# Kernel optimization log

Hardware: AMD Instinct MI355X
Metric: run time of the kernel (lower is better)

Reference implementation:

```python
import math
import jax, jax.numpy as jnp
import numpy as np

B, L, DIM, H = 2, 2048, 1024, 16
D = DIM // H  # head_dim = 64
EPS = 1e-6


def setup_inputs() -> dict:
    key = jax.random.key(0)
    ks = jax.random.split(key, 5)
    s = 0.02
    return {
        "x": jax.random.normal(ks[0], (B, L, DIM), jnp.float32),
        "pe": jax.random.normal(ks[1], (B, 1, L, D // 2, 2, 2), jnp.float32),
        "w_qkv": jax.random.normal(ks[2], (DIM, 3 * DIM), jnp.float32) * s,
        "q_scale": jnp.ones((D,), jnp.float32),
        "k_scale": jnp.ones((D,), jnp.float32),
        "w_proj": jax.random.normal(ks[3], (DIM, DIM), jnp.float32) * s,
        "b_proj": jnp.zeros((DIM,), jnp.float32),
    }


def _rmsnorm(t, scale):
    # flax nnx.RMSNorm: x * rsqrt(mean(x^2) + eps) * scale, over last dim
    var = jnp.mean(jnp.square(t), axis=-1, keepdims=True)
    return t * jax.lax.rsqrt(var + EPS) * scale


def _apply_rope(t, pe):
    # t: [B,H,L,D]; pe: [B,1,L,D/2,2,2]
    t2 = t.reshape(*t.shape[:-1], D // 2, 1, 2)
    out = pe[..., 0] * t2[..., 0] + pe[..., 1] * t2[..., 1]  # [B,H,L,D/2,2]
    return out.reshape(t.shape)


def reference(x, pe, w_qkv, q_scale, k_scale, w_proj, b_proj):
    # fused QKV projection
    qkv = jnp.einsum('bld,de->ble', x, w_qkv)  # [B,L,3*DIM]
    qkv = qkv.reshape(B, L, 3, H, D).transpose(2, 0, 3, 1, 4)  # [3,B,H,L,D]
    q, k, v = qkv[0], qkv[1], qkv[2]
    # QK RMSNorm
    q = _rmsnorm(q, q_scale)
    k = _rmsnorm(k, k_scale)
    # RoPE via pe
    q = _apply_rope(q, pe)
    k = _apply_rope(k, pe)
    # scaled dot product attention
    scores = jnp.einsum('bhqd,bhkd->bhqk', q, k) / math.sqrt(D)
    attn = jax.nn.softmax(scores, axis=-1)
    o = jnp.einsum('bhqk,bhkd->bhqd', attn, v)  # [B,H,L,D]
    o = o.transpose(0, 2, 1, 3).reshape(B, L, DIM)  # B H L D -> B L (H D)
    # output projection
    return jnp.einsum('bld,de->ble', o, w_proj) + b_proj
```

## Files before the change

### kernel.cpp

```cpp
#include <hip/hip_runtime.h>
#include <math.h>

#define BB 2
#define LL 2048
#define DIMM 1024
#define HH 16
#define DD 64
#define QKV_N 3072

typedef unsigned short u16;
typedef unsigned int u32;
typedef __attribute__((ext_vector_type(8))) short short8;
typedef __attribute__((ext_vector_type(4))) float f32x4;

__device__ __forceinline__ float bf2f(u16 h) {
    unsigned u = ((unsigned)h) << 16;
    return __uint_as_float(u);
}
__device__ __forceinline__ u16 f2bf(float f) {
    unsigned u = __float_as_uint(f);
    u += 0x7fffu + ((u >> 16) & 1u);
    return (u16)(u >> 16);
}
__device__ __forceinline__ u32 pack_bf2(float lo, float hi) {
    u32 a = __float_as_uint(hi) + 0x8000u;
    u32 b = __float_as_uint(lo) + 0x8000u;
    return __builtin_amdgcn_perm(a, b, 0x07060302u);
}
__device__ __forceinline__ void gload16(const u16* g, u16* l) {
    __builtin_amdgcn_global_load_lds(
        (const __attribute__((address_space(1))) void*)g,
        (__attribute__((address_space(3))) void*)l, 16, 0, 0);
}

__global__ __launch_bounds__(256) void convx(
    const float* __restrict__ X, u16* __restrict__ Xb)
{
    int i = (blockIdx.x * 256 + threadIdx.x) * 8;
    float4 a = *(const float4*)&X[i];
    float4 b = *(const float4*)&X[i + 4];
    u16 t[8] = {f2bf(a.x), f2bf(a.y), f2bf(a.z), f2bf(a.w),
                f2bf(b.x), f2bf(b.y), f2bf(b.z), f2bf(b.w)};
    *(uint4*)&Xb[i] = *(uint4*)t;
}

__global__ __launch_bounds__(256) void convt(
    const float* __restrict__ W, u16* __restrict__ Wt, int K, int N)
{
    __shared__ u16 s[64][72];
    const int tid = threadIdx.x;
    const int k0 = blockIdx.x * 64, n0 = blockIdx.y * 64;
#pragma unroll
    for (int t = 0; t < 16; ++t) {
        int flat = t * 256 + tid;
        int kk = flat >> 6, nn = flat & 63;
        s[nn][kk] = f2bf(W[(size_t)(k0 + kk) * N + n0 + nn]);
    }
    __syncthreads();
#pragma unroll
    for (int t = 0; t < 2; ++t) {
        int chunk = t * 256 + tid;
        int nn = chunk >> 3, kc = chunk & 7;
        *(uint4*)&Wt[(size_t)(n0 + nn) * K + k0 + kc * 8] = *(uint4*)&s[nn][kc * 8];
    }
}

__global__ __launch_bounds__(256) void gemm_qkv(
    const u16* __restrict__ A, const u16* __restrict__ Bt,
    u16* __restrict__ C, u16* __restrict__ kp, u16* __restrict__ vp,
    const float* __restrict__ pe,
    const float* __restrict__ qs, const float* __restrict__ ks)
{
    __shared__ u16 smem[2 * 16384];

    const int tid = threadIdx.x;
    const int wave = tid >> 6, lane = tid & 63;
    const int mIdx = lane & 15, quad = lane >> 4;
    const int wr = wave >> 1, wc = wave & 1;
    const int xcd = blockIdx.x & 7, lid = blockIdx.x >> 3;
    const int m0 = ((xcd & 3) * 8 + (lid & 7)) * 128;
    const int n0 = ((xcd >> 2) * 12 + (lid >> 3)) * 128;
    const int N = QKV_N, K = DIMM;
    const int lr = lane >> 3, lc = lane & 7;

    f32x4 acc[4][4];
#pragma unroll
    for (int a = 0; a < 4; ++a)
#pragma unroll
        for (int b = 0; b < 4; ++b) acc[a][b] = (f32x4){0.f, 0.f, 0.f, 0.f};

    auto stage = [&](int buf, int k0) {
        u16* sA = smem + buf * 16384;
        u16* sB = sA + 8192;
#pragma unroll
        for (int j = 0; j < 4; ++j) {
            int r0 = 32 * wave + 8 * j + lr;
            int kc = 8 * (lc ^ lr);
            gload16(&A[(size_t)(m0 + r0) * K + k0 + kc], &sA[(32 * wave + 8 * j) * 64]);
            gload16(&Bt[(size_t)(n0 + r0) * K + k0 + kc], &sB[(32 * wave + 8 * j) * 64]);
        }
    };

    stage(0, 0);
    __syncthreads();
    int cur = 0;
    for (int t = 0; t < 16; ++t) {
        if (t + 1 < 16) stage(cur ^ 1, (t + 1) * 64);
        const u16* sA = smem + cur * 16384;
        const u16* sB = sA + 8192;
#pragma unroll
        for (int ks2 = 0; ks2 < 2; ++ks2) {
            short8 af[4], bfr[4];
#pragma unroll
            for (int mt = 0; mt < 4; ++mt) {
                int Ra = 64 * wr + 16 * mt + mIdx;
                af[mt] = *(const short8*)&sA[Ra * 64 + 8 * ((ks2 * 4 + quad) ^ (Ra & 7))];
            }
#pragma unroll
            for (int nt = 0; nt < 4; ++nt) {
                int Rb = 64 * wc + 16 * nt + mIdx;
                bfr[nt] = *(const short8*)&sB[Rb * 64 + 8 * ((ks2 * 4 + quad) ^ (Rb & 7))];
            }
#pragma unroll
            for (int mt = 0; mt < 4; ++mt)
#pragma unroll
                for (int nt = 0; nt < 4; ++nt)
                    acc[mt][nt] = __builtin_amdgcn_mfma_f32_16x16x32_bf16(
                        af[mt], bfr[nt], acc[mt][nt], 0, 0, 0);
        }
        __syncthreads();
        cur ^= 1;
    }

    if (n0 >= 2048) {
#pragma unroll
        for (int mt = 0; mt < 4; ++mt) {
            const int tl0 = 64 * wr + 16 * mt + 4 * quad;
#pragma unroll
            for (int nt = 0; nt < 4; ++nt) {
                const int d = 16 * nt + mIdx;
                const int lblk = ((wc * 2 + (tl0 >> 6)) * 4 + (d >> 4)) * 2
                                 + ((tl0 >> 5) & 1);
                const int ln = (d & 15) + 16 * ((tl0 >> 3) & 3);
                uint2 pr;
                pr.x = pack_bf2(acc[mt][nt][0], acc[mt][nt][1]);
                pr.y = pack_bf2(acc[mt][nt][2], acc[mt][nt][3]);
                *(uint2*)&smem[lblk * 512 + ln * 8 + (tl0 & 7)] = pr;
            }
        }
        __syncthreads();
        {
            const int b = m0 >> 11;
            const int h0 = (n0 - 2048) >> 6;
            const int ktb = (m0 & 2047) >> 6;
#pragma unroll
            for (int g2 = 0; g2 < 4; ++g2) {
                const int bh = b * 16 + h0 + (g2 >> 1);
                const int kt = ktb + (g2 & 1);
                u16* dst = vp + ((size_t)(bh * 32 + kt) * 8) * 512;
                const u16* src = &smem[g2 * 8 * 512];
#pragma unroll
                for (int ps = 0; ps < 2; ++ps) {
                    const int off = (ps * 256 + tid) * 8;
                    *(uint4*)&dst[off] = *(const uint4*)&src[off];
                }
            }
        }
    } else {
        const bool isq = (n0 < 1024);
        const float* scv = isq ? qs : ks;
        const float pre = isq ? 0.18033688011112042f : 1.0f;
        float scl[4];
#pragma unroll
        for (int nt = 0; nt < 4; ++nt) scl[nt] = scv[16 * nt + mIdx];

#pragma unroll
        for (int mt = 0; mt < 4; ++mt) {
#pragma unroll
            for (int r = 0; r < 4; ++r) {
                float s = 0.f;
#pragma unroll
                for (int nt = 0; nt < 4; ++nt) {
                    float a = acc[mt][nt][r];
                    s += a * a;
                }
                s += __shfl_xor(s, 1);
                s += __shfl_xor(s, 2);
                s += __shfl_xor(s, 4);
                s += __shfl_xor(s, 8);
                float rn = rsqrtf(s * (1.f / 64.f) + 1e-6f);
                const int tl = 64 * wr + 16 * mt + 4 * quad + r;
                const int R = m0 + tl;
                size_t peo = (size_t)R * 128;
#pragma unroll
                for (int nt = 0; nt < 4; ++nt) {
                    float v = acc[mt][nt][r] * rn * scl[nt];
                    float pp = __shfl_xor(v, 1);
                    float2 pw = *(const float2*)&pe[peo + 2 * (16 * nt + mIdx)];
                    float e  = (mIdx & 1) ? pp : v;
                    float od = (mIdx & 1) ? v : pp;
                    u16 val = f2bf((pw.x * e + pw.y * od) * pre);
                    if (isq) {
                        C[(size_t)R * N + n0 + 64 * wc + 16 * nt + mIdx] = val;
                    } else {
                        const int d = 16 * nt + mIdx;
                        const int lblk = ((wc * 2 + (tl >> 6)) * 4 + ((tl >> 4) & 3)) * 2
                                         + (d >> 5);
                        smem[lblk * 512 + ((tl & 15) + 16 * ((d >> 3) & 3)) * 8
                             + (d & 7)] = val;
                    }
                }
            }
        }
        if (!isq) {
            __syncthreads();
            const int b = m0 >> 11;
            const int h0 = (n0 - 1024) >> 6;
            const int ktb = (m0 & 2047) >> 6;
#pragma unroll
            for (int g2 = 0; g2 < 4; ++g2) {
                const int bh = b * 16 + h0 + (g2 >> 1);
                const int kt = ktb + (g2 & 1);
                u16* dst = kp + ((size_t)(bh * 32 + kt) * 8) * 512;
                const u16* src = &smem[g2 * 8 * 512];
#pragma unroll
                for (int ps = 0; ps < 2; ++ps) {
                    const int off = (ps * 256 + tid) * 8;
                    *(uint4*)&dst[off] = *(const uint4*)&src[off];
                }
            }
        }
    }
}

__global__ __launch_bounds__(256) void gemm_proj(
    const u16* __restrict__ A, const u16* __restrict__ Bt,
    const float* __restrict__ bias, float* __restrict__ C)
{
    __shared__ u16 smem[2 * 12288];

    const int tid = threadIdx.x;
    const int wave = tid >> 6, lane = tid & 63;
    const int mIdx = lane & 15, quad = lane >> 4;
    const int wr = wave >> 1, wc = wave & 1;
    const int xcd = blockIdx.x & 7, lid = blockIdx.x >> 3;
    const int m0 = (xcd * 8 + (lid >> 3)) * 64;
    const int n0 = (lid & 7) * 128;
    const int N = DIMM, K = DIMM;
    const int lr = lane >> 3, lc = lane & 7;

    f32x4 acc[2][4];
#pragma unroll
    for (int a = 0; a < 2; ++a)
#pragma unroll
        for (int b = 0; b < 4; ++b) acc[a][b] = (f32x4){0.f, 0.f, 0.f, 0.f};

    auto stage = [&](int buf, int k0) {
        u16* sA = smem + buf * 12288;
        u16* sB = sA + 4096;
#pragma unroll
        for (int j = 0; j < 2; ++j) {
            int r0 = 16 * wave + 8 * j + lr;
            gload16(&A[(size_t)(m0 + r0) * K + k0 + 8 * (lc ^ lr)],
                    &sA[(16 * wave + 8 * j) * 64]);
        }
#pragma unroll
        for (int j = 0; j < 4; ++j) {
            int r0 = 32 * wave + 8 * j + lr;
            gload16(&Bt[(size_t)(n0 + r0) * K + k0 + 8 * (lc ^ lr)],
                    &sB[(32 * wave + 8 * j) * 64]);
        }
    };

    stage(0, 0);
    __syncthreads();
    int cur = 0;
    for (int t = 0; t < 16; ++t) {
        if (t + 1 < 16) stage(cur ^ 1, (t + 1) * 64);
        const u16* sA = smem + cur * 12288;
        const u16* sB = sA + 4096;
#pragma unroll
        for (int ks2 = 0; ks2 < 2; ++ks2) {
            short8 af[2], bfr[4];
#pragma unroll
            for (int mt = 0; mt < 2; ++mt) {
                int Ra = 32 * wr + 16 * mt + mIdx;
                af[mt] = *(const short8*)&sA[Ra * 64 + 8 * ((ks2 * 4 + quad) ^ (Ra & 7))];
            }
#pragma unroll
            for (int nt = 0; nt < 4; ++nt) {
                int Rb = 64 * wc + 16 * nt + mIdx;
                bfr[nt] = *(const short8*)&sB[Rb * 64 + 8 * ((ks2 * 4 + quad) ^ (Rb & 7))];
            }
#pragma unroll
            for (int mt = 0; mt < 2; ++mt)
#pragma unroll
                for (int nt = 0; nt < 4; ++nt)
                    acc[mt][nt] = __builtin_amdgcn_mfma_f32_16x16x32_bf16(
                        af[mt], bfr[nt], acc[mt][nt], 0, 0, 0);
        }
        __syncthreads();
        cur ^= 1;
    }

#pragma unroll
    for (int mt = 0; mt < 2; ++mt)
#pragma unroll
        for (int r = 0; r < 4; ++r) {
            int row = m0 + 32 * wr + 16 * mt + quad * 4 + r;
#pragma unroll
            for (int nt = 0; nt < 4; ++nt) {
                int col = n0 + 64 * wc + 16 * nt + mIdx;
                C[(size_t)row * N + col] = acc[mt][nt][r] + bias[col];
            }
        }
}

__global__ __launch_bounds__(256, 2) void attn_mfma(
    const u16* __restrict__ qkv, const u16* __restrict__ kp,
    const u16* __restrict__ vp, u16* __restrict__ o)
{
    __shared__ u16 sP[128 * 64];

    const int tid = threadIdx.x;
    const int wave = tid >> 6;
    const int lane = tid & 63;
    const int mIdx = lane & 15;
    const int quad = lane >> 4;
    const int m7 = mIdx & 7;

    const int bid = ((blockIdx.x & 7) << 6) | (blockIdx.x >> 3);
    const int bh = bid >> 4;
    const int qt = bid & 15;
    const int b = bh >> 4, h = bh & 15;
    const int q0 = qt * 128;

    const u16* kbase = kp + (size_t)bh * 32 * 4096 + lane * 8;
    const u16* vbase = vp + (size_t)bh * 32 * 4096 + lane * 8;

    short8 aq[2][2];
#pragma unroll
    for (int g = 0; g < 2; ++g) {
        const u16* qrow = qkv + (size_t)b * LL * QKV_N + h * 64
                          + (size_t)(q0 + 32 * wave + 16 * g + mIdx) * QKV_N;
        aq[g][0] = *(const short8*)&qrow[quad * 8];
        aq[g][1] = *(const short8*)&qrow[32 + quad * 8];
    }

    const short8 bones = {(short)0x3F80, (short)0x3F80, (short)0x3F80, (short)0x3F80,
                          (short)0x3F80, (short)0x3F80, (short)0x3F80, (short)0x3F80};

    f32x4 Oacc[2][4];
    f32x4 lac[2];
#pragma unroll
    for (int g = 0; g < 2; ++g) {
        lac[g] = (f32x4){0.f, 0.f, 0.f, 0.f};
#pragma unroll
        for (int nb = 0; nb < 4; ++nb) Oacc[g][nb] = (f32x4){0.f, 0.f, 0.f, 0.f};
    }

    const int o0 = 8 * (quad ^ m7);
    const int o1 = 8 * ((quad + 4) ^ m7);
    u16* sPr0 = &sP[(32 * wave + mIdx) * 64];
    u16* sPr1 = &sP[(32 * wave + 16 + mIdx) * 64];

    short8 kfA[8], kfB[8], vf[8];

#pragma unroll
    for (int f = 0; f < 8; ++f) kfA[f] = *(const short8*)&kbase[f * 512];

    auto body = [&](short8* KC, short8* KN, int kt) {
        const size_t tb = (size_t)kt * 4096;
#pragma unroll
        for (int f = 0; f < 8; ++f) vf[f] = *(const short8*)&vbase[tb + f * 512];
        if (kt < 31) {
#pragma unroll
            for (int f = 0; f < 8; ++f) KN[f] = *(const short8*)&kbase[tb + 4096 + f * 512];
        }
        __builtin_amdgcn_sched_barrier(0);

#pragma unroll
        for (int nb = 0; nb < 4; ++nb) {
            const int pofs = (16 * nb + 4 * quad) ^ (8 * m7);
#pragma unroll
            for (int g = 0; g < 2; ++g) {
                f32x4 st = (f32x4){0.f, 0.f, 0.f, 0.f};
                st = __builtin_amdgcn_mfma_f32_16x16x32_bf16(KC[nb * 2 + 0], aq[g][0], st, 0, 0, 0);
                st = __builtin_amdgcn_mfma_f32_16x16x32_bf16(KC[nb * 2 + 1], aq[g][1], st, 0, 0, 0);
                float p0 = exp2f(st[0]), p1 = exp2f(st[1]);
                float p2 = exp2f(st[2]), p3 = exp2f(st[3]);
                uint2 wp;
                wp.x = pack_bf2(p0, p1);
                wp.y = pack_bf2(p2, p3);
                *(uint2*)&((g == 0 ? sPr0 : sPr1)[pofs]) = wp;
            }
        }
        short8 pa00 = *(const short8*)&sPr0[o0];
        short8 pa01 = *(const short8*)&sPr0[o1];
        short8 pa10 = *(const short8*)&sPr1[o0];
        short8 pa11 = *(const short8*)&sPr1[o1];

        lac[0] = __builtin_amdgcn_mfma_f32_16x16x32_bf16(pa00, bones, lac[0], 0, 0, 0);
        lac[0] = __builtin_amdgcn_mfma_f32_16x16x32_bf16(pa01, bones, lac[0], 0, 0, 0);
        lac[1] = __builtin_amdgcn_mfma_f32_16x16x32_bf16(pa10, bones, lac[1], 0, 0, 0);
        lac[1] = __builtin_amdgcn_mfma_f32_16x16x32_bf16(pa11, bones, lac[1], 0, 0, 0);

        __builtin_amdgcn_s_setprio(1);
#pragma unroll
        for (int nb = 0; nb < 4; ++nb) {
            Oacc[0][nb] = __builtin_amdgcn_mfma_f32_16x16x32_bf16(pa00, vf[nb * 2 + 0], Oacc[0][nb], 0, 0, 0);
            Oacc[0][nb] = __builtin_amdgcn_mfma_f32_16x16x32_bf16(pa01, vf[nb * 2 + 1], Oacc[0][nb], 0, 0, 0);
            Oacc[1][nb] = __builtin_amdgcn_mfma_f32_16x16x32_bf16(pa10, vf[nb * 2 + 0], Oacc[1][nb], 0, 0, 0);
            Oacc[1][nb] = __builtin_amdgcn_mfma_f32_16x16x32_bf16(pa11, vf[nb * 2 + 1], Oacc[1][nb], 0, 0, 0);
        }
        __builtin_amdgcn_s_setprio(0);
    };

    for (int kt2 = 0; kt2 < 16; ++kt2) {
        body(kfA, kfB, 2 * kt2);
        body(kfB, kfA, 2 * kt2 + 1);
    }

#pragma unroll
    for (int g = 0; g < 2; ++g)
#pragma unroll
        for (int r = 0; r < 4; ++r) {
            float linv = 1.f / lac[g][r];
            const int rowg = b * LL + q0 + 32 * wave + 16 * g + quad * 4 + r;
#pragma unroll
            for (int nb = 0; nb < 4; ++nb) {
                o[(size_t)rowg * DIMM + h * 64 + 16 * nb + mIdx] =
                    f2bf(Oacc[g][nb][r] * linv);
            }
        }
}

extern "C" void kernel_launch(void* const* d_in, const int* in_sizes, int n_in,
                              void* d_out, int out_size, void* d_ws, size_t ws_size,
                              hipStream_t stream) {
    const float* x       = (const float*)d_in[0];
    const float* pe      = (const float*)d_in[1];
    const float* w_qkv   = (const float*)d_in[2];
    const float* q_scale = (const float*)d_in[3];
    const float* k_scale = (const float*)d_in[4];
    const float* w_proj  = (const float*)d_in[5];
    const float* b_proj  = (const float*)d_in[6];
    float* out = (float*)d_out;

    char* ws = (char*)d_ws;
    u16* qkv    = (u16*)ws;  ws += (size_t)4096 * 3072 * 2;
    u16* o      = (u16*)ws;  ws += (size_t)4096 * 1024 * 2;
    u16* xb     = (u16*)ws;  ws += (size_t)4096 * 1024 * 2;
    u16* wqkvt  = (u16*)ws;  ws += (size_t)3072 * 1024 * 2;
    u16* wprojt = (u16*)ws;  ws += (size_t)1024 * 1024 * 2;
    u16* kpack  = (u16*)ws;  ws += (size_t)32 * 32 * 4096 * 2;
    u16* vpack  = (u16*)ws;  ws += (size_t)32 * 32 * 4096 * 2;

    convx<<<(4096 * 1024) / (256 * 8), 256, 0, stream>>>(x, xb);
    convt<<<dim3(1024 / 64, QKV_N / 64), 256, 0, stream>>>(w_qkv, wqkvt, DIMM, QKV_N);
    convt<<<dim3(1024 / 64, 1024 / 64), 256, 0, stream>>>(w_proj, wprojt, DIMM, DIMM);

    gemm_qkv<<<768, 256, 0, stream>>>(
        xb, wqkvt, qkv, kpack, vpack, pe, q_scale, k_scale);

    attn_mfma<<<BB * HH * (LL / 128), 256, 0, stream>>>(qkv, kpack, vpack, o);

    gemm_proj<<<512, 256, 0, stream>>>(o, wprojt, b_proj, out);
}
```

Before: 231.5 us.

## Pre-pack QKV GEMM operands into MFMA fragment layout and load directly to registers

The conversion kernels now write x and w_qkv in a fragment-major layout matching the MFMA operand order, so each lane reads a contiguous 16-byte short8 per fragment. The QKV GEMM drops the LDS staging and its barriers, loading fragments straight from global memory into registers with a two-stage register double buffer that sched_barriers keep interleaved with MFMAs. This removes LDS traffic and synchronisation, but waves no longer share tiles through LDS, so global/L2 read traffic rises and load latency is exposed more directly. LDS usage falls to one buffer, which is still needed for the epilogue.

```diff
diff --git a/kernel.cpp b/kernel.cpp
--- a/kernel.cpp
+++ b/kernel.cpp
@@ -34,18 +34,25 @@
 }
 
 __global__ __launch_bounds__(256) void convx(
-    const float* __restrict__ X, u16* __restrict__ Xb)
+    const float* __restrict__ X, u16* __restrict__ Af)
 {
-    int i = (blockIdx.x * 256 + threadIdx.x) * 8;
-    float4 a = *(const float4*)&X[i];
-    float4 b = *(const float4*)&X[i + 4];
+    const int g = blockIdx.x * 256 + threadIdx.x;
+    const int lane = g & 63;
+    const int frag = g >> 6;
+    const int rt = frag >> 5;
+    const int kts = (frag >> 1) & 15;
+    const int ks2 = frag & 1;
+    const int R = rt * 16 + (lane & 15);
+    const int k = kts * 64 + ks2 * 32 + ((lane >> 4) & 3) * 8;
+    float4 a = *(const float4*)&X[(size_t)R * DIMM + k];
+    float4 b = *(const float4*)&X[(size_t)R * DIMM + k + 4];
     u16 t[8] = {f2bf(a.x), f2bf(a.y), f2bf(a.z), f2bf(a.w),
                 f2bf(b.x), f2bf(b.y), f2bf(b.z), f2bf(b.w)};
-    *(uint4*)&Xb[i] = *(uint4*)t;
+    *(uint4*)&Af[(size_t)frag * 512 + lane * 8] = *(uint4*)t;
 }
 
 __global__ __launch_bounds__(256) void convt(
-    const float* __restrict__ W, u16* __restrict__ Wt, int K, int N)
+    const float* __restrict__ W, u16* __restrict__ Wt, int K, int N, int fragmode)
 {
     __shared__ u16 s[64][72];
     const int tid = threadIdx.x;
@@ -57,21 +64,37 @@
         s[nn][kk] = f2bf(W[(size_t)(k0 + kk) * N + n0 + nn]);
     }
     __syncthreads();
-#pragma unroll
-    for (int t = 0; t < 2; ++t) {
-        int chunk = t * 256 + tid;
-        int nn = chunk >> 3, kc = chunk & 7;
-        *(uint4*)&Wt[(size_t)(n0 + nn) * K + k0 + kc * 8] = *(uint4*)&s[nn][kc * 8];
+    if (fragmode) {
+        const int kts = k0 >> 6;
+        const int kdiv = K >> 6;
+#pragma unroll
+        for (int t2 = 0; t2 < 2; ++t2) {
+            int idx = t2 * 256 + tid;
+            int fpart = idx >> 6, lane_s = idx & 63;
+            int ct = (n0 >> 4) + (fpart >> 1);
+            int ks2 = fpart & 1;
+            int nn = (fpart >> 1) * 16 + (lane_s & 15);
+            int kk = ks2 * 32 + ((lane_s >> 4) & 3) * 8;
+            *(uint4*)&Wt[((size_t)(ct * kdiv + kts) * 2 + ks2) * 512 + lane_s * 8]
+                = *(const uint4*)&s[nn][kk];
+        }
+    } else {
+#pragma unroll
+        for (int t2 = 0; t2 < 2; ++t2) {
+            int chunk = t2 * 256 + tid;
+            int nn = chunk >> 3, kc = chunk & 7;
+            *(uint4*)&Wt[(size_t)(n0 + nn) * K + k0 + kc * 8] = *(uint4*)&s[nn][kc * 8];
+        }
     }
 }
 
 __global__ __launch_bounds__(256) void gemm_qkv(
-    const u16* __restrict__ A, const u16* __restrict__ Bt,
+    const u16* __restrict__ Af, const u16* __restrict__ Bf,
     u16* __restrict__ C, u16* __restrict__ kp, u16* __restrict__ vp,
     const float* __restrict__ pe,
     const float* __restrict__ qs, const float* __restrict__ ks)
 {
-    __shared__ u16 smem[2 * 16384];
+    __shared__ u16 smem[16384];
 
     const int tid = threadIdx.x;
     const int wave = tid >> 6, lane = tid & 63;
@@ -80,8 +103,10 @@
     const int xcd = blockIdx.x & 7, lid = blockIdx.x >> 3;
     const int m0 = ((xcd & 3) * 8 + (lid & 7)) * 128;
     const int n0 = ((xcd >> 2) * 12 + (lid >> 3)) * 128;
-    const int N = QKV_N, K = DIMM;
-    const int lr = lane >> 3, lc = lane & 7;
+    const int N = QKV_N;
+
+    const u16* abase = Af + ((size_t)((m0 >> 4) + 4 * wr)) * 16384 + lane * 8;
+    const u16* bbase = Bf + ((size_t)((n0 >> 4) + 4 * wc)) * 16384 + lane * 8;
 
     f32x4 acc[4][4];
 #pragma unroll
@@ -89,47 +114,44 @@
 #pragma unroll
         for (int b = 0; b < 4; ++b) acc[a][b] = (f32x4){0.f, 0.f, 0.f, 0.f};
 
-    auto stage = [&](int buf, int k0) {
-        u16* sA = smem + buf * 16384;
-        u16* sB = sA + 8192;
-#pragma unroll
-        for (int j = 0; j < 4; ++j) {
-            int r0 = 32 * wave + 8 * j + lr;
-            int kc = 8 * (lc ^ lr);
-            gload16(&A[(size_t)(m0 + r0) * K + k0 + kc], &sA[(32 * wave + 8 * j) * 64]);
-            gload16(&Bt[(size_t)(n0 + r0) * K + k0 + kc], &sB[(32 * wave + 8 * j) * 64]);
-        }
-    };
-
-    stage(0, 0);
-    __syncthreads();
-    int cur = 0;
+    short8 aA[4], bA[4], aB[4], bB[4];
+#pragma unroll
+    for (int i = 0; i < 4; ++i) {
+        aA[i] = *(const short8*)&abase[(size_t)i * 16384];
+        bA[i] = *(const short8*)&bbase[(size_t)i * 16384];
+    }
+
     for (int t = 0; t < 16; ++t) {
-        if (t + 1 < 16) stage(cur ^ 1, (t + 1) * 64);
-        const u16* sA = smem + cur * 16384;
-        const u16* sB = sA + 8192;
-#pragma unroll
-        for (int ks2 = 0; ks2 < 2; ++ks2) {
-            short8 af[4], bfr[4];
-#pragma unroll
-            for (int mt = 0; mt < 4; ++mt) {
-                int Ra = 64 * wr + 16 * mt + mIdx;
-                af[mt] = *(const short8*)&sA[Ra * 64 + 8 * ((ks2 * 4 + quad) ^ (Ra & 7))];
-            }
-#pragma unroll
-            for (int nt = 0; nt < 4; ++nt) {
-                int Rb = 64 * wc + 16 * nt + mIdx;
-                bfr[nt] = *(const short8*)&sB[Rb * 64 + 8 * ((ks2 * 4 + quad) ^ (Rb & 7))];
-            }
-#pragma unroll
-            for (int mt = 0; mt < 4; ++mt)
-#pragma unroll
-                for (int nt = 0; nt < 4; ++nt)
-                    acc[mt][nt] = __builtin_amdgcn_mfma_f32_16x16x32_bf16(
-                        af[mt], bfr[nt], acc[mt][nt], 0, 0, 0);
-        }
-        __syncthreads();
-        cur ^= 1;
+        const size_t o1 = (size_t)t * 1024 + 512;
+#pragma unroll
+        for (int i = 0; i < 4; ++i) {
+            aB[i] = *(const short8*)&abase[(size_t)i * 16384 + o1];
+            bB[i] = *(const short8*)&bbase[(size_t)i * 16384 + o1];
+        }
+        __builtin_amdgcn_sched_barrier(0);
+#pragma unroll
+        for (int mt = 0; mt < 4; ++mt)
+#pragma unroll
+            for (int nt = 0; nt < 4; ++nt)
+                acc[mt][nt] = __builtin_amdgcn_mfma_f32_16x16x32_bf16(
+                    aA[mt], bA[nt], acc[mt][nt], 0, 0, 0);
+        __builtin_amdgcn_sched_barrier(0);
+        if (t + 1 < 16) {
+            const size_t o0 = (size_t)(t + 1) * 1024;
+#pragma unroll
+            for (int i = 0; i < 4; ++i) {
+                aA[i] = *(const short8*)&abase[(size_t)i * 16384 + o0];
+                bA[i] = *(const short8*)&bbase[(size_t)i * 16384 + o0];
+            }
+        }
+        __builtin_amdgcn_sched_barrier(0);
+#pragma unroll
+        for (int mt = 0; mt < 4; ++mt)
+#pragma unroll
+            for (int nt = 0; nt < 4; ++nt)
+                acc[mt][nt] = __builtin_amdgcn_mfma_f32_16x16x32_bf16(
+                    aB[mt], bB[nt], acc[mt][nt], 0, 0, 0);
+        __builtin_amdgcn_sched_barrier(0);
     }
 
     if (n0 >= 2048) {
@@ -457,8 +479,8 @@
     u16* vpack  = (u16*)ws;  ws += (size_t)32 * 32 * 4096 * 2;
 
     convx<<<(4096 * 1024) / (256 * 8), 256, 0, stream>>>(x, xb);
-    convt<<<dim3(1024 / 64, QKV_N / 64), 256, 0, stream>>>(w_qkv, wqkvt, DIMM, QKV_N);
-    convt<<<dim3(1024 / 64, 1024 / 64), 256, 0, stream>>>(w_proj, wprojt, DIMM, DIMM);
+    convt<<<dim3(1024 / 64, QKV_N / 64), 256, 0, stream>>>(w_qkv, wqkvt, DIMM, QKV_N, 1);
+    convt<<<dim3(1024 / 64, 1024 / 64), 256, 0, stream>>>(w_proj, wprojt, DIMM, DIMM, 0);
 
     gemm_qkv<<<768, 256, 0, stream>>>(
         xb, wqkvt, qkv, kpack, vpack, pe, q_scale, k_scale);
```

Result: faster. 221.4 us (-4.4%).
